# Kernel optimization log

Measured on AMD Instinct MI355X. Metric: run time of the kernel, lower is better.

## Reference

```python
import jax, jax.numpy as jnp
import numpy as np

B, T, H = 2, 2048, 2048
E, K, I = 8, 2, 1408


def setup_inputs() -> dict:
    key = jax.random.key(0)
    ks = jax.random.split(key, 6)
    x = jax.random.normal(ks[0], (B, T, H), dtype=jnp.float32)
    # router: small-std, row-normalized init (as in the torch module)
    gw = jax.random.normal(ks[1], (E, H), dtype=jnp.float32) * 1e-3
    gw = gw / (jnp.linalg.norm(gw, axis=-1, keepdims=True) + 1e-6)
    scale1 = 1.0 / np.sqrt(H)
    scale2 = 1.0 / np.sqrt(I)
    W1 = jax.random.normal(ks[2], (E, H, I), dtype=jnp.float32) * scale1  # fc1 per expert
    W2 = jax.random.normal(ks[3], (E, I, H), dtype=jnp.float32) * scale2  # fc2 per expert
    Ws1 = jax.random.normal(ks[4], (H, I), dtype=jnp.float32) * scale1    # shared expert fc1
    Ws2 = jax.random.normal(ks[5], (I, H), dtype=jnp.float32) * scale2    # shared expert fc2
    return {"x": x, "gate_w": gw, "W1": W1, "W2": W2, "Ws1": Ws1, "Ws2": Ws2}


def reference(x, gate_w, W1, W2, Ws1, Ws2):
    b, t, h = x.shape
    nt = b * t
    x_flat = x.reshape(nt, h)

    # router
    gate_logits = x_flat @ gate_w.T                       # [nt, E]
    gate_probs = jax.nn.softmax(gate_logits.astype(jnp.float32), axis=-1)
    topk_vals, topk_idx = jax.lax.top_k(gate_probs, K)    # [nt, K]

    # aux (load-balancing) loss
    importance = gate_probs.mean(axis=0)                  # [E]
    load = jnp.zeros((E,), jnp.float32).at[topk_idx.reshape(-1)].add(1.0)
    load = load / (nt * K)
    aux_loss = (importance * load).sum() * E

    # combine weights: zero except at top-k experts (NOT renormalized, matching forward)
    combine = jnp.sum(jax.nn.one_hot(topk_idx, E, dtype=jnp.float32)
                      * topk_vals[..., None], axis=1)     # [nt, E]

    # dense expert compute (equivalent to gather-expert-scatter with 0 weights elsewhere)
    h1 = jnp.einsum('th,ehi->tei', x_flat, W1)            # [nt, E, I]
    h1 = h1 * jax.nn.sigmoid(h1)                          # SiLU
    expert_out = jnp.einsum('tei,eih->teh', h1, W2)       # [nt, E, H]
    y_flat = jnp.einsum('teh,te->th', expert_out, combine)

    # shared expert (always on)
    hs = x_flat @ Ws1
    y_flat = y_flat + (hs * jax.nn.sigmoid(hs)) @ Ws2

    y = y_flat.reshape(b, t, h).astype(x.dtype)
    return y, aux_loss
```

## Files before the change

kernel.cpp:

```cpp
#include <hip/hip_runtime.h>
#include <hip/hip_bf16.h>

#define NT 4096
#define HD 2048
#define NE 8
#define TOPK 2
#define ID 1408
#define NG 9
#define BM 128
#define BN 64
#define BK 64
#define MT_MAX 104

typedef unsigned short u16;
typedef unsigned int u32;
typedef unsigned long long u64;
typedef __attribute__((ext_vector_type(8))) short bf16x8;
typedef __attribute__((ext_vector_type(4))) float f32x4;

__device__ __forceinline__ u16 f2bf(float f) {
    u32 u = __builtin_bit_cast(u32, f);
    u += 0x7FFFu + ((u >> 16) & 1u);
    return (u16)(u >> 16);
}
__device__ __forceinline__ float bflo(u32 v) { return __builtin_bit_cast(float, v << 16); }
__device__ __forceinline__ float bfhi(u32 v) { return __builtin_bit_cast(float, v & 0xffff0000u); }

typedef __attribute__((address_space(1))) const void gas_void;
typedef __attribute__((address_space(3))) void las_void;
__device__ __forceinline__ void gl_lds16(const void* g, void* l) {
    __builtin_amdgcn_global_load_lds((gas_void*)(u64)g, (las_void*)(u32)(u64)l, 16, 0, 0);
}

__global__ void router_tw1_kernel(const float* __restrict__ x, const float* __restrict__ gw,
                                  int* __restrict__ counts, float* __restrict__ imp,
                                  int* __restrict__ tki, float* __restrict__ tkv,
                                  u16* __restrict__ xb,
                                  const float* __restrict__ W1, const float* __restrict__ Ws1,
                                  u16* __restrict__ wt1) {
    __shared__ float s_imp[NE];
    __shared__ int s_cnt[NE];
    __shared__ u16 Lt[64][68];
    int tid = threadIdx.x;
    if (blockIdx.x < NT / 4) {
        if (tid < NE) { s_imp[tid] = 0.f; s_cnt[tid] = 0; }
        int w = tid >> 6, lane = tid & 63;
        int t = blockIdx.x * 4 + w;
        float acc[NE];
#pragma unroll
        for (int e = 0; e < NE; e++) acc[e] = 0.f;
        const float* xr = x + (size_t)t * HD;
        u16* xw = xb + (size_t)t * HD;
#pragma unroll
        for (int i = 0; i < 4; i++) {
            int cc = i * 64 + lane;
            int b64 = cc >> 3, j = cc & 7, h = j >> 2, q = j & 3;
            int k0 = b64 * 64 + h * 32 + q * 4;
            float4 v0 = *(const float4*)(xr + k0);
            float4 v1 = *(const float4*)(xr + k0 + 16);
#pragma unroll
            for (int e = 0; e < NE; e++) {
                const float* gp = gw + e * HD + k0;
                float4 g0 = *(const float4*)(gp);
                float4 g1 = *(const float4*)(gp + 16);
                acc[e] += v0.x * g0.x + v0.y * g0.y + v0.z * g0.z + v0.w * g0.w
                        + v1.x * g1.x + v1.y * g1.y + v1.z * g1.z + v1.w * g1.w;
            }
            ushort4 o0, o1;
            o0.x = f2bf(v0.x); o0.y = f2bf(v0.y); o0.z = f2bf(v0.z); o0.w = f2bf(v0.w);
            o1.x = f2bf(v1.x); o1.y = f2bf(v1.y); o1.z = f2bf(v1.z); o1.w = f2bf(v1.w);
            uint4 o;
            o.x = (u32)o0.x | ((u32)o0.y << 16); o.y = (u32)o0.z | ((u32)o0.w << 16);
            o.z = (u32)o1.x | ((u32)o1.y << 16); o.w = (u32)o1.z | ((u32)o1.w << 16);
            *(uint4*)(xw + b64 * 64 + j * 8) = o;
        }
#pragma unroll
        for (int e = 0; e < NE; e++) {
#pragma unroll
            for (int o = 32; o >= 1; o >>= 1) acc[e] += __shfl_xor(acc[e], o, 64);
        }
        __syncthreads();
        if (lane == 0) {
            float mx = acc[0];
            for (int e = 1; e < NE; e++) mx = fmaxf(mx, acc[e]);
            float p[NE], sum = 0.f;
            for (int e = 0; e < NE; e++) { p[e] = expf(acc[e] - mx); sum += p[e]; }
            float inv = 1.f / sum;
            for (int e = 0; e < NE; e++) p[e] *= inv;
            int i1 = 0;
            for (int e = 1; e < NE; e++) if (p[e] > p[i1]) i1 = e;
            int i2 = (i1 == 0) ? 1 : 0;
            for (int e = 0; e < NE; e++) if (e != i1 && p[e] > p[i2]) i2 = e;
            tki[t * 2 + 0] = i1; tkv[t * 2 + 0] = p[i1];
            tki[t * 2 + 1] = i2; tkv[t * 2 + 1] = p[i2];
            for (int e = 0; e < NE; e++) atomicAdd(&s_imp[e], p[e]);
            atomicAdd(&s_cnt[i1], 1); atomicAdd(&s_cnt[i2], 1);
        }
        __syncthreads();
        if (tid < NE) {
            atomicAdd(&imp[tid], s_imp[tid]);
            atomicAdd(&counts[tid], s_cnt[tid]);
        }
    } else {
        int tw = blockIdx.x - NT / 4;
        int e = tw / 704, rem = tw % 704;
        int n0 = (rem % 22) * 64, k0 = (rem / 22) * 64;
        const float* src = (e < NE) ? (W1 + (size_t)e * HD * ID) : Ws1;
        u16* dst = wt1 + (size_t)e * ID * HD;
#pragma unroll
        for (int i = 0; i < 4; i++) {
            int idx = i * 256 + tid;
            int kl = idx >> 4, nq = (idx & 15) * 4;
            float4 v = *(const float4*)(src + (size_t)(k0 + kl) * ID + n0 + nq);
            Lt[nq + 0][kl] = f2bf(v.x); Lt[nq + 1][kl] = f2bf(v.y);
            Lt[nq + 2][kl] = f2bf(v.z); Lt[nq + 3][kl] = f2bf(v.w);
        }
        __syncthreads();
#pragma unroll
        for (int c2 = 0; c2 < 2; c2++) {
            int cid = tid * 2 + c2;
            int nr = cid >> 3, j = cid & 7;
            int h = j >> 2, q = j & 3;
            int kb = h * 32 + q * 4;
            uint2 lo = *(const uint2*)&Lt[nr][kb];
            uint2 hi = *(const uint2*)&Lt[nr][kb + 16];
            uint4 o; o.x = lo.x; o.y = lo.y; o.z = hi.x; o.w = hi.y;
            *(uint4*)(dst + (size_t)(n0 + nr) * HD + k0 + j * 8) = o;
        }
    }
}

__global__ void prepscat_kernel(const int* __restrict__ counts, const float* __restrict__ imp,
                                int* __restrict__ off, int* __restrict__ tileoff,
                                float* __restrict__ out_aux,
                                int* __restrict__ tki, const float* __restrict__ tkv,
                                int* __restrict__ list, float* __restrict__ wgt) {
    __shared__ int s_off[NG];
    __shared__ int s_cur[NE];
    int tid = threadIdx.x;
    if (tid == 0) {
        int o = 0, to = 0;
        for (int g = 0; g < NG; g++) {
            int c = (g < NE) ? counts[g] : NT;
            off[g] = o; s_off[g] = o; tileoff[g] = to;
            o += c; to += (c + BM - 1) / BM;
        }
        off[NG] = o; tileoff[NG] = to;
        float aux = 0.f;
        for (int e = 0; e < NE; e++)
            aux += (imp[e] / (float)NT) * ((float)counts[e] / (float)(NT * TOPK));
        *out_aux = aux * (float)NE;
    }
    if (tid < NE) s_cur[tid] = 0;
    __syncthreads();
    for (int t = tid; t < NT; t += 256) {
#pragma unroll
        for (int k = 0; k < TOPK; k++) {
            int e = tki[t * 2 + k];
            int pos = atomicAdd(&s_cur[e], 1);
            int s = s_off[e] + pos;
            list[s] = t;
            wgt[s] = tkv[t * 2 + k];
            tki[t * 2 + k] = s;
        }
        list[s_off[NE] + t] = t;
        wgt[s_off[NE] + t] = 1.0f;
    }
}

__global__ void transw_kernel(const float* __restrict__ W, const float* __restrict__ Wsh,
                              u16* __restrict__ dst, int K, int N) {
    int e = blockIdx.z;
    const float* src = (e < NE) ? (W + (size_t)e * K * N) : Wsh;
    dst += (size_t)e * N * K;
    int k0 = blockIdx.y * 64, n0 = blockIdx.x * 64;
    __shared__ u16 Lt[64][68];
    int tid = threadIdx.x;
#pragma unroll
    for (int i = 0; i < 4; i++) {
        int idx = i * 256 + tid;
        int kl = idx >> 4, nq = (idx & 15) * 4;
        float4 v = *(const float4*)(src + (size_t)(k0 + kl) * N + n0 + nq);
        Lt[nq + 0][kl] = f2bf(v.x); Lt[nq + 1][kl] = f2bf(v.y);
        Lt[nq + 2][kl] = f2bf(v.z); Lt[nq + 3][kl] = f2bf(v.w);
    }
    __syncthreads();
#pragma unroll
    for (int c2 = 0; c2 < 2; c2++) {
        int cid = tid * 2 + c2;
        int nr = cid >> 3, j = cid & 7;
        int h = j >> 2, q = j & 3;
        int kb = h * 32 + q * 4;
        uint2 lo = *(const uint2*)&Lt[nr][kb];
        uint2 hi = *(const uint2*)&Lt[nr][kb + 16];
        uint4 o; o.x = lo.x; o.y = lo.y; o.z = hi.x; o.w = hi.y;
        *(uint4*)(dst + (size_t)(n0 + nr) * K + k0 + j * 8) = o;
    }
}

__global__ __launch_bounds__(256) void fc1_kernel(
    const u16* __restrict__ xb, const u16* __restrict__ Wt1,
    const int* __restrict__ off, const int* __restrict__ tileoff,
    const int* __restrict__ list, u16* __restrict__ h1) {
    __shared__ u16 S[2 * 12288];
    int nwg = gridDim.x * gridDim.y;
    int orig = blockIdx.y * gridDim.x + blockIdx.x;
    int wg = (orig & 7) * (nwg >> 3) + (orig >> 3);
    int bx = wg % gridDim.x, mt = wg / gridDim.x;

    int g = -1, gto = 0;
#pragma unroll
    for (int gg = 0; gg < NG; gg++)
        if (mt >= tileoff[gg] && mt < tileoff[gg + 1]) { g = gg; gto = tileoff[gg]; }
    if (g < 0) return;
    int goff = off[g], cnt = off[g + 1] - goff;
    int row0 = (mt - gto) * BM;
    const u16* Wb = Wt1 + (size_t)g * (ID * HD);
    int n0 = bx * BN;
    int tid = threadIdx.x, lane = tid & 63, w = tid >> 6;
    int lm = lane >> 3;
    int lc = (((lane & 7) ^ lm) << 3);
    const u16* pa[4]; const u16* pb[2];
#pragma unroll
    for (int i = 0; i < 4; i++) {
        int c = i * 4 + w;
        int r = row0 + c * 8 + lm;
        r = (r < cnt) ? r : (cnt - 1);
        pa[i] = xb + (size_t)list[goff + r] * HD + lc;
    }
#pragma unroll
    for (int i = 0; i < 2; i++) {
        int c = i * 4 + w;
        pb[i] = Wb + (size_t)(n0 + c * 8 + lm) * HD + lc;
    }
    int wr = w >> 1, wc = w & 1;
    int lr = lane & 15, l7 = lane & 7, q2 = lane >> 4;
    f32x4 acc[4][2] = {};

    auto stage = [&](int b) {
        u16* A = S + b * 12288;
        u16* B = A + 8192;
#pragma unroll
        for (int i = 0; i < 4; i++) { gl_lds16(pa[i], A + (i * 4 + w) * 512); pa[i] += BK; }
#pragma unroll
        for (int i = 0; i < 2; i++) { gl_lds16(pb[i], B + (i * 4 + w) * 512); pb[i] += BK; }
    };
    auto compute = [&](int b) {
        const u16* A = S + b * 12288;
        const u16* B = A + 8192;
#pragma unroll
        for (int kc = 0; kc < 8; kc += 4) {
            int slot = ((kc + q2) ^ l7) << 3;
            bf16x8 a[4], bb[2];
#pragma unroll
            for (int f = 0; f < 4; f++)
                a[f] = __builtin_bit_cast(bf16x8, *(const uint4*)&A[(wr * 64 + f * 16 + lr) * BK + slot]);
#pragma unroll
            for (int f = 0; f < 2; f++)
                bb[f] = __builtin_bit_cast(bf16x8, *(const uint4*)&B[(wc * 32 + f * 16 + lr) * BK + slot]);
            __builtin_amdgcn_s_setprio(1);
#pragma unroll
            for (int mf = 0; mf < 4; mf++)
#pragma unroll
                for (int nf = 0; nf < 2; nf++)
                    acc[mf][nf] = __builtin_amdgcn_mfma_f32_16x16x32_bf16(a[mf], bb[nf], acc[mf][nf], 0, 0, 0);
            __builtin_amdgcn_s_setprio(0);
        }
    };

    stage(0);
    int cur = 0;
    for (int t = 1; t < HD / BK; ++t) {
        stage(cur ^ 1);
        asm volatile("s_waitcnt vmcnt(6)" ::: "memory");
        __builtin_amdgcn_s_barrier();
        compute(cur);
        asm volatile("s_waitcnt lgkmcnt(0)" ::: "memory");
        __builtin_amdgcn_s_barrier();
        cur ^= 1;
    }
    asm volatile("s_waitcnt vmcnt(0)" ::: "memory");
    __builtin_amdgcn_s_barrier();
    compute(cur);

    int q4 = q2 * 4;
    int cl = ((lr >> 2) << 3) + (lr & 3);
#pragma unroll
    for (int mf = 0; mf < 4; mf++)
#pragma unroll
        for (int reg = 0; reg < 4; reg++) {
            int r = row0 + wr * 64 + mf * 16 + q4 + reg;
            if (r < cnt) {
                size_t rb = (size_t)(goff + r) * ID + n0;
#pragma unroll
                for (int nf = 0; nf < 2; nf++) {
                    float v = acc[mf][nf][reg];
                    h1[rb + wc * 32 + (nf << 2) + cl] = f2bf(v / (1.f + __expf(-v)));
                }
            }
        }
}

template <bool EO>
__global__ __launch_bounds__(256) void fc2_kernel(
    const u16* __restrict__ h1, const u16* __restrict__ Wt2,
    const int* __restrict__ off, const int* __restrict__ tileoff,
    const int* __restrict__ list, const float* __restrict__ wgt,
    u16* __restrict__ eo, float* __restrict__ y) {
    __shared__ u16 S[2 * 12288];
    int nwg = gridDim.x * gridDim.y;
    int orig = blockIdx.y * gridDim.x + blockIdx.x;
    int wg = (orig & 7) * (nwg >> 3) + (orig >> 3);
    int bx = wg % gridDim.x, mt = wg / gridDim.x;

    int g = -1, gto = 0;
#pragma unroll
    for (int gg = 0; gg < NG; gg++)
        if (mt >= tileoff[gg] && mt < tileoff[gg + 1]) { g = gg; gto = tileoff[gg]; }
    if (g < 0) return;
    int goff = off[g], cnt = off[g + 1] - goff;
    int row0 = (mt - gto) * BM;
    const u16* Wb = Wt2 + (size_t)g * (ID * HD);
    int n0 = bx * BN;
    int tid = threadIdx.x, lane = tid & 63, w = tid >> 6;
    int lm = lane >> 3;
    int lc = (((lane & 7) ^ lm) << 3);
    const u16* pa[4]; const u16* pb[2];
#pragma unroll
    for (int i = 0; i < 4; i++) {
        int c = i * 4 + w;
        int r = row0 + c * 8 + lm;
        r = (r < cnt) ? r : (cnt - 1);
        pa[i] = h1 + (size_t)(goff + r) * ID + lc;
    }
#pragma unroll
    for (int i = 0; i < 2; i++) {
        int c = i * 4 + w;
        pb[i] = Wb + (size_t)(n0 + c * 8 + lm) * ID + lc;
    }
    int wr = w >> 1, wc = w & 1;
    int lr = lane & 15, l7 = lane & 7, q2 = lane >> 4;
    f32x4 acc[4][2] = {};

    auto stage = [&](int b) {
        u16* A = S + b * 12288;
        u16* B = A + 8192;
#pragma unroll
        for (int i = 0; i < 4; i++) { gl_lds16(pa[i], A + (i * 4 + w) * 512); pa[i] += BK; }
#pragma unroll
        for (int i = 0; i < 2; i++) { gl_lds16(pb[i], B + (i * 4 + w) * 512); pb[i] += BK; }
    };
    auto compute = [&](int b) {
        const u16* A = S + b * 12288;
        const u16* B = A + 8192;
#pragma unroll
        for (int kc = 0; kc < 8; kc += 4) {
            int slot = ((kc + q2) ^ l7) << 3;
            bf16x8 a[4], bb[2];
#pragma unroll
            for (int f = 0; f < 4; f++)
                a[f] = __builtin_bit_cast(bf16x8, *(const uint4*)&A[(wr * 64 + f * 16 + lr) * BK + slot]);
#pragma unroll
            for (int f = 0; f < 2; f++)
                bb[f] = __builtin_bit_cast(bf16x8, *(const uint4*)&B[(wc * 32 + f * 16 + lr) * BK + slot]);
            __builtin_amdgcn_s_setprio(1);
#pragma unroll
            for (int mf = 0; mf < 4; mf++)
#pragma unroll
                for (int nf = 0; nf < 2; nf++)
                    acc[mf][nf] = __builtin_amdgcn_mfma_f32_16x16x32_bf16(a[mf], bb[nf], acc[mf][nf], 0, 0, 0);
            __builtin_amdgcn_s_setprio(0);
        }
    };

    stage(0);
    int cur = 0;
    for (int t = 1; t < ID / BK; ++t) {
        stage(cur ^ 1);
        asm volatile("s_waitcnt vmcnt(6)" ::: "memory");
        __builtin_amdgcn_s_barrier();
        compute(cur);
        asm volatile("s_waitcnt lgkmcnt(0)" ::: "memory");
        __builtin_amdgcn_s_barrier();
        cur ^= 1;
    }
    asm volatile("s_waitcnt vmcnt(0)" ::: "memory");
    __builtin_amdgcn_s_barrier();
    compute(cur);

    int q4 = q2 * 4;
#pragma unroll
    for (int mf = 0; mf < 4; mf++)
#pragma unroll
        for (int reg = 0; reg < 4; reg++) {
            int r = row0 + wr * 64 + mf * 16 + q4 + reg;
            if (r < cnt) {
                int slot = goff + r;
                if (EO) {
                    size_t rb = (size_t)slot * HD + n0 + wc * 32;
#pragma unroll
                    for (int nf = 0; nf < 2; nf++)
                        eo[rb + nf * 16 + lr] = f2bf(acc[mf][nf][reg]);
                } else {
                    int tok = list[slot];
                    float wv = wgt[slot];
                    float* yr = y + (size_t)tok * HD + n0 + wc * 32;
#pragma unroll
                    for (int nf = 0; nf < 2; nf++)
                        atomicAdd(yr + nf * 16 + lr, acc[mf][nf][reg] * wv);
                }
            }
        }
}

__global__ __launch_bounds__(256) void combine_kernel(
    const u16* __restrict__ eo, const int* __restrict__ smap,
    const float* __restrict__ tkv, const int* __restrict__ off,
    float* __restrict__ y) {
    int idx = blockIdx.x * 256 + threadIdx.x;
    int t = idx >> 8;
    int cc = (idx & 255) << 3;
    int s0 = smap[t * 2 + 0], s1 = smap[t * 2 + 1];
    float w0 = tkv[t * 2 + 0], w1 = tkv[t * 2 + 1];
    int s2 = off[NE] + t;
    uint4 A = *(const uint4*)(eo + (size_t)s0 * HD + cc);
    uint4 B = *(const uint4*)(eo + (size_t)s1 * HD + cc);
    uint4 C = *(const uint4*)(eo + (size_t)s2 * HD + cc);
    float4 o0, o1;
    o0.x = w0 * bflo(A.x) + w1 * bflo(B.x) + bflo(C.x);
    o0.y = w0 * bfhi(A.x) + w1 * bfhi(B.x) + bfhi(C.x);
    o0.z = w0 * bflo(A.y) + w1 * bflo(B.y) + bflo(C.y);
    o0.w = w0 * bfhi(A.y) + w1 * bfhi(B.y) + bfhi(C.y);
    o1.x = w0 * bflo(A.z) + w1 * bflo(B.z) + bflo(C.z);
    o1.y = w0 * bfhi(A.z) + w1 * bfhi(B.z) + bfhi(C.z);
    o1.z = w0 * bflo(A.w) + w1 * bflo(B.w) + bflo(C.w);
    o1.w = w0 * bfhi(A.w) + w1 * bfhi(B.w) + bfhi(C.w);
    float* yr = y + (size_t)t * HD + cc;
    *(float4*)yr = o0;
    *(float4*)(yr + 4) = o1;
}

extern "C" void kernel_launch(void* const* d_in, const int* in_sizes, int n_in,
                              void* d_out, int out_size, void* d_ws, size_t ws_size,
                              hipStream_t stream) {
    const float* x   = (const float*)d_in[0];
    const float* gw  = (const float*)d_in[1];
    const float* W1  = (const float*)d_in[2];
    const float* W2  = (const float*)d_in[3];
    const float* Ws1 = (const float*)d_in[4];
    const float* Ws2 = (const float*)d_in[5];
    float* out = (float*)d_out;

    char* ws = (char*)d_ws;
    int*   counts  = (int*)(ws + 0);
    int*   off     = (int*)(ws + 128);
    int*   tileoff = (int*)(ws + 192);
    float* imp     = (float*)(ws + 256);
    int*   tki     = (int*)(ws + 320);
    float* tkv     = (float*)(ws + 33088);
    int*   list    = (int*)(ws + 65856);
    float* wgt     = (float*)(ws + 115008);
    u16* xb  = (u16*)(ws + 164352);
    u16* wt1 = (u16*)(ws + 16941568ULL);
    u16* h1  = (u16*)(ws + 68846080ULL);
    u16* wt2 = (u16*)(ws + 164352);
    u16* eo  = (u16*)(ws + 103449088ULL);
    const bool use_eo = (ws_size >= 153780736ULL);

    if (!use_eo)
        hipMemsetAsync(d_out, 0, (size_t)out_size * sizeof(float), stream);
    hipMemsetAsync(d_ws, 0, 320, stream);

    router_tw1_kernel<<<NT / 4 + 6336, 256, 0, stream>>>(
        x, gw, counts, imp, tki, tkv, xb, W1, Ws1, wt1);
    prepscat_kernel<<<1, 256, 0, stream>>>(
        counts, imp, off, tileoff, out + (size_t)NT * HD, tki, tkv, list, wgt);

    fc1_kernel<<<dim3(ID / BN, MT_MAX), 256, 0, stream>>>(xb, wt1, off, tileoff, list, h1);

    transw_kernel<<<dim3(HD / 64, ID / 64, NG), 256, 0, stream>>>(W2, Ws2, wt2, ID, HD);

    if (use_eo) {
        fc2_kernel<true><<<dim3(HD / BN, MT_MAX), 256, 0, stream>>>(
            h1, wt2, off, tileoff, list, wgt, eo, out);
        combine_kernel<<<NT, 256, 0, stream>>>(eo, tki, tkv, off, out);
    } else {
        fc2_kernel<false><<<dim3(HD / BN, MT_MAX), 256, 0, stream>>>(
            h1, wt2, off, tileoff, list, wgt, eo, out);
    }
}
```

Baseline: 311.1 us.

## Fuse W2 transpose-convert into fc1 launch as extra workgroups when workspace allows

```diff
diff --git a/kernel.cpp b/kernel.cpp
--- a/kernel.cpp
+++ b/kernel.cpp
@@ -11,6 +11,8 @@
 #define BN 64
 #define BK 64
 #define MT_MAX 104
+#define NWG1 2288
+#define NTW 6336
 
 typedef unsigned short u16;
 typedef unsigned int u32;
@@ -198,15 +200,48 @@
     }
 }
 
+template <bool FTW>
 __global__ __launch_bounds__(256) void fc1_kernel(
     const u16* __restrict__ xb, const u16* __restrict__ Wt1,
     const int* __restrict__ off, const int* __restrict__ tileoff,
-    const int* __restrict__ list, u16* __restrict__ h1) {
+    const int* __restrict__ list, u16* __restrict__ h1,
+    const float* __restrict__ W2, const float* __restrict__ Ws2,
+    u16* __restrict__ wt2) {
     __shared__ u16 S[2 * 12288];
-    int nwg = gridDim.x * gridDim.y;
-    int orig = blockIdx.y * gridDim.x + blockIdx.x;
-    int wg = (orig & 7) * (nwg >> 3) + (orig >> 3);
-    int bx = wg % gridDim.x, mt = wg / gridDim.x;
+    int wg0 = blockIdx.x;
+    int tid = threadIdx.x;
+    if (FTW && wg0 >= NWG1) {
+        u16 (*Lt)[68] = (u16(*)[68])S;
+        int tw = wg0 - NWG1;
+        int e = tw / 704, rem = tw % 704;
+        int n0 = (rem % 32) * 64, k0 = (rem / 32) * 64;
+        const float* src = (e < NE) ? (W2 + (size_t)e * ID * HD) : Ws2;
+        u16* dst = wt2 + (size_t)e * HD * ID;
+#pragma unroll
+        for (int i = 0; i < 4; i++) {
+            int idx = i * 256 + tid;
+            int kl = idx >> 4, nq = (idx & 15) * 4;
+            float4 v = *(const float4*)(src + (size_t)(k0 + kl) * HD + n0 + nq);
+            Lt[nq + 0][kl] = f2bf(v.x); Lt[nq + 1][kl] = f2bf(v.y);
+            Lt[nq + 2][kl] = f2bf(v.z); Lt[nq + 3][kl] = f2bf(v.w);
+        }
+        __syncthreads();
+#pragma unroll
+        for (int c2 = 0; c2 < 2; c2++) {
+            int cid = tid * 2 + c2;
+            int nr = cid >> 3, j = cid & 7;
+            int h = j >> 2, q = j & 3;
+            int kb = h * 32 + q * 4;
+            uint2 lo = *(const uint2*)&Lt[nr][kb];
+            uint2 hi = *(const uint2*)&Lt[nr][kb + 16];
+            uint4 o; o.x = lo.x; o.y = lo.y; o.z = hi.x; o.w = hi.y;
+            *(uint4*)(dst + (size_t)(n0 + nr) * ID + k0 + j * 8) = o;
+        }
+        return;
+    }
+    int orig = wg0;
+    int wg = (orig & 7) * (NWG1 >> 3) + (orig >> 3);
+    int bx = wg % (ID / BN), mt = wg / (ID / BN);
 
     int g = -1, gto = 0;
 #pragma unroll
@@ -217,7 +252,7 @@
     int row0 = (mt - gto) * BM;
     const u16* Wb = Wt1 + (size_t)g * (ID * HD);
     int n0 = bx * BN;
-    int tid = threadIdx.x, lane = tid & 63, w = tid >> 6;
+    int lane = tid & 63, w = tid >> 6;
     int lm = lane >> 3;
     int lc = (((lane & 7) ^ lm) << 3);
     const u16* pa[4]; const u16* pb[2];
@@ -463,22 +498,28 @@
     u16* xb  = (u16*)(ws + 164352);
     u16* wt1 = (u16*)(ws + 16941568ULL);
     u16* h1  = (u16*)(ws + 68846080ULL);
-    u16* wt2 = (u16*)(ws + 164352);
     u16* eo  = (u16*)(ws + 103449088ULL);
-    const bool use_eo = (ws_size >= 153780736ULL);
+    const bool use_big = (ws_size >= 205685248ULL);
+    const bool use_eo  = (ws_size >= 153780736ULL);
+    u16* wt2 = use_big ? (u16*)(ws + 153780736ULL) : (u16*)(ws + 164352);
 
     if (!use_eo)
         hipMemsetAsync(d_out, 0, (size_t)out_size * sizeof(float), stream);
     hipMemsetAsync(d_ws, 0, 320, stream);
 
-    router_tw1_kernel<<<NT / 4 + 6336, 256, 0, stream>>>(
+    router_tw1_kernel<<<NT / 4 + NTW, 256, 0, stream>>>(
         x, gw, counts, imp, tki, tkv, xb, W1, Ws1, wt1);
     prepscat_kernel<<<1, 256, 0, stream>>>(
         counts, imp, off, tileoff, out + (size_t)NT * HD, tki, tkv, list, wgt);
 
-    fc1_kernel<<<dim3(ID / BN, MT_MAX), 256, 0, stream>>>(xb, wt1, off, tileoff, list, h1);
-
-    transw_kernel<<<dim3(HD / 64, ID / 64, NG), 256, 0, stream>>>(W2, Ws2, wt2, ID, HD);
+    if (use_big) {
+        fc1_kernel<true><<<NWG1 + NTW, 256, 0, stream>>>(
+            xb, wt1, off, tileoff, list, h1, W2, Ws2, wt2);
+    } else {
+        fc1_kernel<false><<<NWG1, 256, 0, stream>>>(
+            xb, wt1, off, tileoff, list, h1, W2, Ws2, wt2);
+        transw_kernel<<<dim3(HD / 64, ID / 64, NG), 256, 0, stream>>>(W2, Ws2, wt2, ID, HD);
+    }
 
     if (use_eo) {
         fc2_kernel<true><<<dim3(HD / BN, MT_MAX), 256, 0, stream>>>(
```

Result: no change. 305.4 us (-1.8%).
